# Kernel optimization log

Hardware: AMD Instinct MI355X
Metric: run time of the kernel (lower is better)

Reference implementation:

```python
import jax, jax.numpy as jnp
import numpy as np

B, C, N, K = 2, 128, 8192, 16
DL = 128  # dim_L; Fourier half-dim = 64; mlp hidden = 32


def setup_inputs() -> dict:
    key = jax.random.key(0)
    ks = jax.random.split(key, 16)
    s = 0.05
    return {
        "x": jax.random.normal(ks[0], (B, C, N, 1), jnp.float32),
        "coords": jax.random.normal(ks[1], (B, N, 4), jnp.float32),
        "idx": jax.random.randint(ks[2], (B, N, K), 0, N, jnp.int64),
        "B_gauss": jax.random.normal(ks[3], (4, DL // 2), jnp.float32),
        "W1": jax.random.normal(ks[4], (DL, DL // 4), jnp.float32) * s,
        "b1": jax.random.normal(ks[5], (DL // 4,), jnp.float32) * s,
        "W2": jax.random.normal(ks[6], (DL // 4, C), jnp.float32) * s,
        "b2": jax.random.normal(ks[7], (C,), jnp.float32) * s,
        "Wq": jax.random.normal(ks[8], (C, C), jnp.float32) * s,
        "bq": jax.random.normal(ks[9], (C,), jnp.float32) * s,
        "Wk": jax.random.normal(ks[10], (C, C), jnp.float32) * s,
        "bk": jax.random.normal(ks[11], (C,), jnp.float32) * s,
        "Wv": jax.random.normal(ks[12], (C, C), jnp.float32) * s,
        "bv": jax.random.normal(ks[13], (C,), jnp.float32) * s,
        "Wo": jax.random.normal(ks[14], (C, C), jnp.float32) * s,
        "bo": jax.random.normal(ks[15], (C,), jnp.float32) * s,
    }


def reference(x, coords, idx, B_gauss, W1, b1, W2, b2, Wq, bq, Wk, bk, Wv, bv, Wo, bo):
    xs = x[..., 0]  # [B, C, N]
    # gather neighbor coords/features via KNN idx (vmapped over batch)
    nb_coords = jax.vmap(lambda c, i: c[i])(coords, idx)          # [B, N, K, 4]
    nb_feats = jax.vmap(lambda f, i: f[:, i])(xs, idx)            # [B, C, N, K]
    delta_p = nb_coords - coords[:, :, None, :]                   # [B, N, K, 4]
    # random-Fourier geometric embedding
    proj = jnp.matmul(delta_p, B_gauss)                           # [B, N, K, DL/2]
    two_pi = 2.0 * jnp.pi
    E_freq = jnp.concatenate([jnp.sin(two_pi * proj), jnp.cos(two_pi * proj)], axis=-1)
    h = jax.nn.relu(E_freq @ W1 + b1) @ W2 + b2                   # [B, N, K, C]
    E_geo = jnp.transpose(h, (0, 3, 1, 2))                        # [B, C, N, K]
    # 1x1 conv projections == channel matmuls (PyTorch conv weight acts as out<-in)
    Q = jnp.einsum('oc,bcn->bon', Wq, xs) + bq[None, :, None]     # [B, C, N]
    KV_in = nb_feats + E_geo                                      # [B, C, N, K]
    Kt = jnp.einsum('oc,bcnk->bonk', Wk, KV_in) + bk[None, :, None, None]
    Vt = jnp.einsum('oc,bcnk->bonk', Wv, KV_in) + bv[None, :, None, None]
    # local dot-product attention over K neighbors
    attn = jnp.sum(Q[..., None] * Kt, axis=1, keepdims=True) / jnp.sqrt(jnp.float32(C))
    attn = jax.nn.softmax(attn, axis=-1)                          # [B, 1, N, K]
    out = jnp.sum(attn * Vt, axis=-1, keepdims=True)              # [B, C, N, 1]
    out = jnp.einsum('oc,bcnk->bonk', Wo, out) + bo[None, :, None, None]
    return out
```

## Files before the change

### kernel.cpp

```cpp
#include <hip/hip_runtime.h>


using u16 = unsigned short;
using u32 = unsigned int;
using u64 = unsigned long long;

typedef short bf16x8 __attribute__((ext_vector_type(8)));
typedef float f32x4  __attribute__((ext_vector_type(4)));

__device__ __forceinline__ float bl(u32 u) { return __uint_as_float(u << 16); }
__device__ __forceinline__ float bh(u32 u) { return __uint_as_float(u & 0xffff0000u); }
__device__ __forceinline__ float b2f(u16 u) { return __uint_as_float(((u32)u) << 16); }
__device__ __forceinline__ u16 f2b(float f) {
    u32 u = __float_as_uint(f);
    u32 r = u + 0x7fffu + ((u >> 16) & 1u);
    return (u16)(r >> 16);
}
__device__ __forceinline__ float dot8(uint4 wv, const float* xp) {
    float4 a = *(const float4*)xp;
    float4 b = *(const float4*)(xp + 4);
    return bl(wv.x)*a.x + bh(wv.x)*a.y + bl(wv.y)*a.z + bh(wv.y)*a.w
         + bl(wv.z)*b.x + bh(wv.z)*b.y + bl(wv.w)*b.z + bh(wv.w)*b.w;
}
__device__ __forceinline__ u64 pack4(float a, float b, float c, float d) {
    return (u64)f2b(a) | ((u64)f2b(b) << 16) | ((u64)f2b(c) << 32) | ((u64)f2b(d) << 48);
}
__device__ __forceinline__ int fidxA(int m, int c) {
    return (((m >> 4)*4 + (c >> 5))*64 + ((c >> 3) & 3)*16 + (m & 15))*8 + (c & 7);
}

__global__ void __launch_bounds__(512)
k_pt(const float* __restrict__ x,
     const float* __restrict__ Wq, const float* __restrict__ bq,
     const float* __restrict__ Wk, const float* __restrict__ bk,
     const float* __restrict__ Wv, const float* __restrict__ bv,
     const float* __restrict__ Wo, const float* __restrict__ bo,
     const float* __restrict__ W1, const float* __restrict__ W2,
     u16* __restrict__ Afrag, u16* __restrict__ Wovfrag,
     u16* __restrict__ W1frag, u16* __restrict__ W2frag,
     u16* __restrict__ W2Tfrag,
     float* __restrict__ bA, float* __restrict__ su,
     float* __restrict__ bov, float* __restrict__ d0,
     u16* __restrict__ xT)
{
    const int blk = blockIdx.x, tid = threadIdx.x;

    if (blk >= 130) {
        __shared__ u16 tile[32][33];
        const int blk2 = blk - 130;
        const int b  = blk2 >> 10;
        const int ct = (blk2 >> 8) & 3;
        const int nt = blk2 & 255;
        const int tx = tid & 31, ty = tid >> 5;
        const size_t xb = (size_t)b * 128 * 8192;
        #pragma unroll
        for (int j = 0; j < 2; ++j) {
            int c = ct*32 + ty + j*16;
            tile[ty + j*16][tx] = f2b(x[xb + (size_t)c * 8192 + (size_t)(nt*32 + tx)]);
        }
        __syncthreads();
        #pragma unroll
        for (int j = 0; j < 2; ++j) {
            int n = nt*32 + ty + j*16;
            xT[xb + (size_t)n * 128 + (size_t)(ct*32 + tx)] = tile[tx][ty + j*16];
        }
        return;
    }

    const int i = tid & 127, p = tid >> 7;
    if (blk < 128) {
        __shared__ float sWk[128], sWo[128];
        __shared__ float s_pA[4][128], s_pV[4][128];
        if (tid < 128) sWk[tid] = Wk[tid*128 + blk];
        else if (tid < 256) sWo[tid-128] = Wo[blk*128 + (tid-128)];
        __syncthreads();
        float accA = 0.f, accV = 0.f;
        #pragma unroll 8
        for (int o = p*32; o < p*32 + 32; ++o) {
            accA += sWk[o] * Wq[o*128 + i];
            accV += sWo[o] * Wv[o*128 + i];
        }
        s_pA[p][i] = accA; s_pV[p][i] = accV;
        __syncthreads();
        if (tid < 128) {
            float v = s_pA[0][tid] + s_pA[1][tid] + s_pA[2][tid] + s_pA[3][tid];
            Afrag[fidxA(blk, tid)] = f2b(v);
        } else if (tid < 256) {
            int ii = tid - 128;
            float v = s_pV[0][ii] + s_pV[1][ii] + s_pV[2][ii] + s_pV[3][ii];
            Wovfrag[fidxA(blk, ii)] = f2b(v);
        }
    } else if (blk == 128) {
        __shared__ float s_r[3][4][128];
        float a1 = 0.f, a2 = 0.f, a3 = 0.f;
        #pragma unroll 8
        for (int o = p*32; o < p*32 + 32; ++o) {
            a1 += Wk[o*128 + i] * bq[o];
            a2 += Wq[o*128 + i] * bk[o];
            a3 += Wo[i*128 + o] * bv[o];
        }
        s_r[0][p][i] = a1; s_r[1][p][i] = a2; s_r[2][p][i] = a3;
        __syncthreads();
        if (tid < 128) {
            bA[tid] = s_r[0][0][tid] + s_r[0][1][tid] + s_r[0][2][tid] + s_r[0][3][tid];
        } else if (tid < 256) {
            int ii = tid - 128;
            su[ii] = s_r[1][0][ii] + s_r[1][1][ii] + s_r[1][2][ii] + s_r[1][3][ii];
        } else if (tid < 384) {
            int ii = tid - 256;
            bov[ii] = s_r[2][0][ii] + s_r[2][1][ii] + s_r[2][2][ii] + s_r[2][3][ii] + bo[ii];
        } else if (tid < 448) {
            int l = tid - 384;
            float part = bq[l]*bk[l] + bq[l+64]*bk[l+64];
            part += __shfl_xor(part, 1);
            part += __shfl_xor(part, 2);
            part += __shfl_xor(part, 4);
            part += __shfl_xor(part, 8);
            part += __shfl_xor(part, 16);
            part += __shfl_xor(part, 32);
            if (l == 0) *d0 = part;
        }
    } else {
        for (int e = tid; e < 4096; e += 512) {
            int ii = e & 127, r2 = e >> 7;
            {
                int nt = r2 >> 4, lmm = r2 & 15;
                int ks = ii >> 5, q = (ii >> 3) & 3, j = ii & 7;
                W1frag[((nt*4 + ks)*64 + q*16 + lmm)*8 + j] = f2b(W1[ii*32 + r2]);
            }
            {
                int mt = r2 >> 4, lmm = r2 & 15;
                int ks = ii >> 5, q = (ii >> 3) & 3, j = ii & 7;
                W2frag[((mt*4 + ks)*64 + q*16 + lmm)*8 + j] = f2b(W2[r2*128 + ii]);
            }
            {
                int mt = ii >> 4, lmm = ii & 15;
                int q = r2 >> 3, j = r2 & 7;
                W2Tfrag[(mt*64 + q*16 + lmm)*8 + j] = f2b(W2[r2*128 + ii]);
            }
        }
    }
}

__global__ void __launch_bounds__(256, 4)
k_main(const u16* __restrict__ xT, const float* __restrict__ coords,
       const int* __restrict__ idx, const float* __restrict__ Bg,
       const float* __restrict__ b1g, const float* __restrict__ b2g,
       const u16* __restrict__ Afrag, const u16* __restrict__ Wovfrag,
       const u16* __restrict__ W1frag, const u16* __restrict__ W2frag,
       const u16* __restrict__ W2Tfrag,
       const float* __restrict__ bAg, const float* __restrict__ sug,
       const float* __restrict__ bovg, const float* __restrict__ d0g,
       float* __restrict__ out)
{
    __shared__ __align__(16) u16   sH[128][40];
    __shared__ __align__(16) u16   s_qkb[8][136];
    __shared__ __align__(16) u16   s_gb[8][40];
    __shared__ __align__(16) u16   s_wtb[8][136];
    __shared__ __align__(16) float s_xb[8][132];
    __shared__ __align__(16) float s_del[128][4];
    __shared__ float s_sc[8][17];
    __shared__ float s_attn[8][17];
    __shared__ u16   sHbar[32][12];
    __shared__ float s_e0[8];
    __shared__ __align__(16) float s_b2[128], s_su[128];
    __shared__ float s_bA[128], s_bov[128], s_b1[32];
    __shared__ __align__(16) float sBgT[64][4];
    __shared__ int s_idx[128];

    const int tid = threadIdx.x;
    const int w = tid >> 6, l = tid & 63, lm = l & 15, lq = l >> 4, lmm = lm & 7;
    const int g0 = blockIdx.x * 8;
    const int bsel = g0 >> 13;
    const int n0 = g0 & 8191;
    const size_t bbase = ((size_t)bsel) << 13;
    const float inv_sqrtC = 0.08838834764831845f;

    if (tid < 128) {
        s_bA[tid] = bAg[tid]; s_su[tid] = sug[tid];
        s_bov[tid] = bovg[tid]; s_b2[tid] = b2g[tid];
    } else if (tid < 160) {
        s_b1[tid-128] = b1g[tid-128];
    }
    sBgT[tid >> 2][tid & 3] = Bg[(tid & 3)*64 + (tid >> 2)];
    const float c_d0 = *d0g;

    if (tid < 128) {
        int j = idx[(size_t)g0*16 + tid];
        s_idx[tid] = j;
        float4 cj = *(const float4*)&coords[(size_t)(bbase + j)*4];
        float4 cn = *(const float4*)&coords[(size_t)(g0 + (tid >> 4))*4];
        *(float4*)s_del[tid] = make_float4(cj.x-cn.x, cj.y-cn.y, cj.z-cn.z, cj.w-cn.w);
    }
    f32x4 accq[2] = {{0.f,0.f,0.f,0.f},{0.f,0.f,0.f,0.f}};
    {
        const bf16x8* Af = (const bf16x8*)Afrag;
        bf16x8 bfr[4];
        #pragma unroll
        for (int ks = 0; ks < 4; ++ks)
            bfr[ks] = *(const bf16x8*)&xT[(((size_t)(g0 + lmm)) << 7) + ks*32 + lq*8];
        #pragma unroll
        for (int mi = 0; mi < 2; ++mi) {
            const int ct = w*2 + mi;
            #pragma unroll
            for (int ks = 0; ks < 4; ++ks) {
                bf16x8 a = Af[(ct*4 + ks)*64 + l];
                accq[mi] = __builtin_amdgcn_mfma_f32_16x16x32_bf16(a, bfr[ks], accq[mi], 0, 0, 0);
            }
        }
    }
    __syncthreads();

    if (lm < 8) {
        #pragma unroll
        for (int mi = 0; mi < 2; ++mi) {
            int c0 = (w*2 + mi)*16 + lq*4;
            *(u64*)&s_qkb[lm][c0] = pack4(accq[mi][0] + s_bA[c0],   accq[mi][1] + s_bA[c0+1],
                                          accq[mi][2] + s_bA[c0+2], accq[mi][3] + s_bA[c0+3]);
        }
    }
    __syncthreads();

    {
        const bf16x8* W1f = (const bf16x8*)W1frag;
        bf16x8 w1f[2][4];
        #pragma unroll
        for (int nt = 0; nt < 2; ++nt)
            #pragma unroll
            for (int ks = 0; ks < 4; ++ks) w1f[nt][ks] = W1f[(nt*4 + ks)*64 + l];
        #pragma unroll
        for (int mi = 0; mi < 2; ++mi) {
            const int mt = w*2 + mi;
            float4 d = *(const float4*)s_del[mt*16 + lm];
            bf16x8 ea[4];
            #pragma unroll
            for (int ksp = 0; ksp < 2; ++ksp) {
                #pragma unroll
                for (int jp = 0; jp < 4; ++jp) {
                    int f = ksp*32 + lq*8 + jp*2;
                    float4 ga = *(const float4*)sBgT[f];
                    float4 gb = *(const float4*)sBgT[f+1];
                    float p0 = d.x*ga.x + d.y*ga.y + d.z*ga.z + d.w*ga.w;
                    float p1 = d.x*gb.x + d.y*gb.y + d.z*gb.z + d.w*gb.w;
                    p0 -= floorf(p0); p1 -= floorf(p1);
                    ((u32*)&ea[ksp])[jp]   = (u32)f2b(__builtin_amdgcn_sinf(p0))
                                           | ((u32)f2b(__builtin_amdgcn_sinf(p1)) << 16);
                    ((u32*)&ea[ksp+2])[jp] = (u32)f2b(__builtin_amdgcn_cosf(p0))
                                           | ((u32)f2b(__builtin_amdgcn_cosf(p1)) << 16);
                }
            }
            f32x4 acch[2] = {{0.f,0.f,0.f,0.f},{0.f,0.f,0.f,0.f}};
            #pragma unroll
            for (int ks = 0; ks < 4; ++ks) {
                acch[0] = __builtin_amdgcn_mfma_f32_16x16x32_bf16(ea[ks], w1f[0][ks], acch[0], 0,0,0);
                acch[1] = __builtin_amdgcn_mfma_f32_16x16x32_bf16(ea[ks], w1f[1][ks], acch[1], 0,0,0);
            }
            #pragma unroll
            for (int nt = 0; nt < 2; ++nt) {
                float b1v = s_b1[nt*16 + lm];
                #pragma unroll
                for (int r = 0; r < 4; ++r)
                    sH[mt*16 + lq*4 + r][nt*16 + lm] = f2b(fmaxf(acch[nt][r] + b1v, 0.f));
            }
        }
    }
    if (w < 2) {
        const bf16x8* W2f = (const bf16x8*)W2frag;
        f32x4 accg = {0.f,0.f,0.f,0.f};
        #pragma unroll
        for (int ks = 0; ks < 4; ++ks) {
            bf16x8 a = W2f[(w*4 + ks)*64 + l];
            bf16x8 bv = *(const bf16x8*)&s_qkb[lmm][ks*32 + lq*8];
            accg = __builtin_amdgcn_mfma_f32_16x16x32_bf16(a, bv, accg, 0, 0, 0);
        }
        if (lm < 8) {
            int m0 = w*16 + lq*4;
            *(u64*)&s_gb[lm][m0] = pack4(accg[0], accg[1], accg[2], accg[3]);
        }
    } else {
        int t = tid - 128;
        if (t < 64) {
            int n = t >> 3, sub = t & 7, c0 = sub*16;
            uint4 q0 = *(const uint4*)&s_qkb[n][c0];
            uint4 q1 = *(const uint4*)&s_qkb[n][c0+8];
            uint4 x0 = *(const uint4*)&xT[(((size_t)(g0 + n)) << 7) + c0];
            uint4 x1 = *(const uint4*)&xT[(((size_t)(g0 + n)) << 7) + c0 + 8];
            float part = dot8(q0, &s_b2[c0]) + dot8(q1, &s_b2[c0+8])
                       + dot8(x0, &s_su[c0]) + dot8(x1, &s_su[c0+8]);
            part += __shfl_xor(part, 1);
            part += __shfl_xor(part, 2);
            part += __shfl_xor(part, 4);
            if (sub == 0) s_e0[n] = part + c_d0;
        }
    }
    __syncthreads();

    {
        bf16x8 bq4[5];
        #pragma unroll
        for (int ks = 0; ks < 4; ++ks) bq4[ks] = *(const bf16x8*)&s_qkb[lmm][ks*32 + lq*8];
        bq4[4] = *(const bf16x8*)&s_gb[lmm][lq*8];
        #pragma unroll
        for (int mi = 0; mi < 2; ++mi) {
            const int mt = w*2 + mi;
            const size_t rb = ((size_t)(bbase + s_idx[mt*16 + lm])) << 7;
            f32x4 acc = {0.f,0.f,0.f,0.f};
            #pragma unroll
            for (int ks = 0; ks < 4; ++ks) {
                bf16x8 a = *(const bf16x8*)&xT[rb + ks*32 + lq*8];
                acc = __builtin_amdgcn_mfma_f32_16x16x32_bf16(a, bq4[ks], acc, 0, 0, 0);
            }
            {
                bf16x8 a = *(const bf16x8*)&sH[mt*16 + lm][lq*8];
                acc = __builtin_amdgcn_mfma_f32_16x16x32_bf16(a, bq4[4], acc, 0, 0, 0);
            }
            if (lm == mt) {
                #pragma unroll
                for (int r = 0; r < 4; ++r) s_sc[mt][lq*4 + r] = acc[r];
            }
        }
    }
    __syncthreads();

    if (tid < 128) {
        int n = tid >> 4, k = tid & 15;
        float s = (s_sc[n][k] + s_e0[n]) * inv_sqrtC;
        float mx = s;
        mx = fmaxf(mx, __shfl_xor(mx, 1, 16));
        mx = fmaxf(mx, __shfl_xor(mx, 2, 16));
        mx = fmaxf(mx, __shfl_xor(mx, 4, 16));
        mx = fmaxf(mx, __shfl_xor(mx, 8, 16));
        float ex = __expf(s - mx);
        float sm = ex;
        sm += __shfl_xor(sm, 1, 16);
        sm += __shfl_xor(sm, 2, 16);
        sm += __shfl_xor(sm, 4, 16);
        sm += __shfl_xor(sm, 8, 16);
        s_attn[n][k] = ex / sm;
    }
    __syncthreads();

    {
        int n = tid >> 5, cs = tid & 31, c0 = cs*4;
        float a0[16];
        #pragma unroll
        for (int k = 0; k < 16; ++k) a0[k] = s_attn[n][k];
        float4 facc = *(const float4*)&s_b2[c0];
        #pragma unroll
        for (int k = 0; k < 16; ++k) {
            uint2 v = *(const uint2*)&xT[(((size_t)(bbase + s_idx[n*16 + k])) << 7) + c0];
            facc.x += a0[k]*bl(v.x); facc.y += a0[k]*bh(v.x);
            facc.z += a0[k]*bl(v.y); facc.w += a0[k]*bh(v.y);
        }
        *(float4*)&s_xb[n][c0] = facc;
        int m = cs;
        float hacc = 0.f;
        #pragma unroll
        for (int k = 0; k < 16; ++k) hacc += a0[k] * b2f(sH[n*16 + k][m]);
        sHbar[m][n] = f2b(hacc);
    }
    __syncthreads();

    {
        const bf16x8* W2Tf = (const bf16x8*)W2Tfrag;
        bf16x8 bv;
        #pragma unroll
        for (int j = 0; j < 8; ++j) bv[j] = (short)sHbar[lq*8 + j][lmm];
        #pragma unroll
        for (int mi = 0; mi < 2; ++mi) {
            const int mt = w*2 + mi;
            bf16x8 a = W2Tf[mt*64 + l];
            f32x4 accw = {0.f,0.f,0.f,0.f};
            accw = __builtin_amdgcn_mfma_f32_16x16x32_bf16(a, bv, accw, 0, 0, 0);
            if (lm < 8) {
                int c0 = mt*16 + lq*4;
                float4 xb4 = *(const float4*)&s_xb[lm][c0];
                *(u64*)&s_wtb[lm][c0] = pack4(xb4.x + accw[0], xb4.y + accw[1],
                                              xb4.z + accw[2], xb4.w + accw[3]);
            }
        }
    }
    __syncthreads();

    {
        const bf16x8* Wvf = (const bf16x8*)Wovfrag;
        bf16x8 bv[4];
        #pragma unroll
        for (int ks = 0; ks < 4; ++ks) bv[ks] = *(const bf16x8*)&s_wtb[lmm][ks*32 + lq*8];
        #pragma unroll
        for (int mi = 0; mi < 2; ++mi) {
            const int ct = w*2 + mi;
            f32x4 acco = {0.f,0.f,0.f,0.f};
            #pragma unroll
            for (int ks = 0; ks < 4; ++ks) {
                bf16x8 a = Wvf[(ct*4 + ks)*64 + l];
                acco = __builtin_amdgcn_mfma_f32_16x16x32_bf16(a, bv[ks], acco, 0, 0, 0);
            }
            if (lm < 8) {
                #pragma unroll
                for (int r = 0; r < 4; ++r) {
                    int o = ct*16 + lq*4 + r;
                    out[(((size_t)(bsel*128 + o)) << 13) + n0 + lm] = acco[r] + s_bov[o];
                }
            }
        }
    }
}

extern "C" void kernel_launch(void* const* d_in, const int* in_sizes, int n_in,
                              void* d_out, int out_size, void* d_ws, size_t ws_size,
                              hipStream_t stream)
{
    const float* x      = (const float*)d_in[0];
    const float* coords = (const float*)d_in[1];
    const int*   idx    = (const int*)d_in[2];
    const float* Bg     = (const float*)d_in[3];
    const float* W1     = (const float*)d_in[4];
    const float* b1     = (const float*)d_in[5];
    const float* W2     = (const float*)d_in[6];
    const float* b2     = (const float*)d_in[7];
    const float* Wq     = (const float*)d_in[8];
    const float* bq     = (const float*)d_in[9];
    const float* Wk     = (const float*)d_in[10];
    const float* bk     = (const float*)d_in[11];
    const float* Wv     = (const float*)d_in[12];
    const float* bv     = (const float*)d_in[13];
    const float* Wo     = (const float*)d_in[14];
    const float* bo     = (const float*)d_in[15];
    float* out = (float*)d_out;

    char* ws = (char*)d_ws;
    u16*   Afrag   = (u16*)(ws);
    u16*   Wovfrag = (u16*)(ws + 32768);
    u16*   W1frag  = (u16*)(ws + 65536);
    u16*   W2frag  = (u16*)(ws + 73728);
    u16*   W2Tfrag = (u16*)(ws + 81920);
    float* bA      = (float*)(ws + 90112);
    float* su      = (float*)(ws + 90624);
    float* bov     = (float*)(ws + 91136);
    float* d0      = (float*)(ws + 91648);
    u16*   xT      = (u16*)(ws + 94208);

    k_pt<<<2178, 512, 0, stream>>>(x, Wq, bq, Wk, bk, Wv, bv, Wo, bo, W1, W2,
                                   Afrag, Wovfrag, W1frag, W2frag, W2Tfrag,
                                   bA, su, bov, d0, xT);
    k_main<<<2048, 256, 0, stream>>>(xT, coords, idx, Bg, b1, b2,
                                     Afrag, Wovfrag, W1frag, W2frag, W2Tfrag,
                                     bA, su, bov, d0, out);
}
```

Before: 128.9 us.

## Fold b2 and W2 into precomputed weights, prefetch neighbor rows, fuse softmax

Bias b2 is folded algebraically into the key-side and output constants, and Wo·Wv is premultiplied with W2 into a new fragment matrix. This removes the separate W2^T MFMA stage and one block-wide barrier in the main kernel. Neighbor feature rows are prefetched into registers at kernel start. Softmax is now computed directly from MFMA accumulators with cross-lane shuffles, dropping the score staging buffer and another barrier. Shared-memory bias staging is replaced by direct global reads, blocks interleave the two batches, and the weighted-sum intermediate is stored in bf16, which adds some rounding error.

```diff
diff --git a/kernel.cpp b/kernel.cpp
--- a/kernel.cpp
+++ b/kernel.cpp
@@ -36,11 +36,12 @@
      const float* __restrict__ Wv, const float* __restrict__ bv,
      const float* __restrict__ Wo, const float* __restrict__ bo,
      const float* __restrict__ W1, const float* __restrict__ W2,
+     const float* __restrict__ b2,
      u16* __restrict__ Afrag, u16* __restrict__ Wovfrag,
      u16* __restrict__ W1frag, u16* __restrict__ W2frag,
-     u16* __restrict__ W2Tfrag,
-     float* __restrict__ bA, float* __restrict__ su,
-     float* __restrict__ bov, float* __restrict__ d0,
+     u16* __restrict__ Wovt2frag,
+     float* __restrict__ bA, float* __restrict__ su2,
+     float* __restrict__ bov2, float* __restrict__ d0b,
      u16* __restrict__ xT)
 {
     const int blk = blockIdx.x, tid = threadIdx.x;
@@ -71,6 +72,7 @@
     if (blk < 128) {
         __shared__ float sWk[128], sWo[128];
         __shared__ float s_pA[4][128], s_pV[4][128];
+        __shared__ float s_row[128];
         if (tid < 128) sWk[tid] = Wk[tid*128 + blk];
         else if (tid < 256) sWo[tid-128] = Wo[blk*128 + (tid-128)];
         __syncthreads();
@@ -89,36 +91,51 @@
             int ii = tid - 128;
             float v = s_pV[0][ii] + s_pV[1][ii] + s_pV[2][ii] + s_pV[3][ii];
             Wovfrag[fidxA(blk, ii)] = f2b(v);
+            s_row[ii] = v;
+        }
+        __syncthreads();
+        if (tid < 32) {
+            float wv2 = 0.f;
+            for (int c = 0; c < 128; ++c) wv2 += s_row[c] * W2[tid*128 + c];
+            Wovt2frag[(((blk >> 4)*64) + (tid >> 3)*16 + (blk & 15))*8 + (tid & 7)] = f2b(wv2);
+        } else if (tid == 32) {
+            float rb2 = 0.f, a3 = 0.f;
+            for (int c = 0; c < 128; ++c) rb2 += s_row[c] * b2[c];
+            for (int o = 0; o < 128; ++o) a3 += sWo[o] * bv[o];
+            bov2[blk] = rb2 + a3 + bo[blk];
         }
     } else if (blk == 128) {
-        __shared__ float s_r[3][4][128];
-        float a1 = 0.f, a2 = 0.f, a3 = 0.f;
+        __shared__ float s_t[128];
+        __shared__ float s_p1[4][128], s_p2[4][128];
+        if (tid < 128) {
+            float tt = 0.f;
+            for (int c = 0; c < 128; ++c) tt += Wk[tid*128 + c] * b2[c];
+            s_t[tid] = tt + bk[tid];
+        }
+        __syncthreads();
+        float a1 = 0.f, a2 = 0.f;
         #pragma unroll 8
         for (int o = p*32; o < p*32 + 32; ++o) {
             a1 += Wk[o*128 + i] * bq[o];
-            a2 += Wq[o*128 + i] * bk[o];
-            a3 += Wo[i*128 + o] * bv[o];
-        }
-        s_r[0][p][i] = a1; s_r[1][p][i] = a2; s_r[2][p][i] = a3;
+            a2 += Wq[o*128 + i] * s_t[o];
+        }
+        s_p1[p][i] = a1; s_p2[p][i] = a2;
         __syncthreads();
         if (tid < 128) {
-            bA[tid] = s_r[0][0][tid] + s_r[0][1][tid] + s_r[0][2][tid] + s_r[0][3][tid];
+            bA[tid] = s_p1[0][tid] + s_p1[1][tid] + s_p1[2][tid] + s_p1[3][tid];
         } else if (tid < 256) {
             int ii = tid - 128;
-            su[ii] = s_r[1][0][ii] + s_r[1][1][ii] + s_r[1][2][ii] + s_r[1][3][ii];
-        } else if (tid < 384) {
-            int ii = tid - 256;
-            bov[ii] = s_r[2][0][ii] + s_r[2][1][ii] + s_r[2][2][ii] + s_r[2][3][ii] + bo[ii];
-        } else if (tid < 448) {
-            int l = tid - 384;
-            float part = bq[l]*bk[l] + bq[l+64]*bk[l+64];
+            su2[ii] = s_p2[0][ii] + s_p2[1][ii] + s_p2[2][ii] + s_p2[3][ii];
+        } else if (tid < 320) {
+            int l = tid - 256;
+            float part = bq[l]*s_t[l] + bq[l+64]*s_t[l+64];
             part += __shfl_xor(part, 1);
             part += __shfl_xor(part, 2);
             part += __shfl_xor(part, 4);
             part += __shfl_xor(part, 8);
             part += __shfl_xor(part, 16);
             part += __shfl_xor(part, 32);
-            if (l == 0) *d0 = part;
+            if (l == 0) *d0b = part;
         }
     } else {
         for (int e = tid; e < 4096; e += 512) {
@@ -133,11 +150,6 @@
                 int ks = ii >> 5, q = (ii >> 3) & 3, j = ii & 7;
                 W2frag[((mt*4 + ks)*64 + q*16 + lmm)*8 + j] = f2b(W2[r2*128 + ii]);
             }
-            {
-                int mt = ii >> 4, lmm = ii & 15;
-                int q = r2 >> 3, j = r2 & 7;
-                W2Tfrag[(mt*64 + q*16 + lmm)*8 + j] = f2b(W2[r2*128 + ii]);
-            }
         }
     }
 }
@@ -145,52 +157,57 @@
 __global__ void __launch_bounds__(256, 4)
 k_main(const u16* __restrict__ xT, const float* __restrict__ coords,
        const int* __restrict__ idx, const float* __restrict__ Bg,
-       const float* __restrict__ b1g, const float* __restrict__ b2g,
+       const float* __restrict__ b1g,
        const u16* __restrict__ Afrag, const u16* __restrict__ Wovfrag,
        const u16* __restrict__ W1frag, const u16* __restrict__ W2frag,
-       const u16* __restrict__ W2Tfrag,
-       const float* __restrict__ bAg, const float* __restrict__ sug,
-       const float* __restrict__ bovg, const float* __restrict__ d0g,
+       const u16* __restrict__ Wovt2frag,
+       const float* __restrict__ bAg, const float* __restrict__ su2g,
+       const float* __restrict__ bov2g, const float* __restrict__ d0bg,
        float* __restrict__ out)
 {
     __shared__ __align__(16) u16   sH[128][40];
     __shared__ __align__(16) u16   s_qkb[8][136];
     __shared__ __align__(16) u16   s_gb[8][40];
-    __shared__ __align__(16) u16   s_wtb[8][136];
-    __shared__ __align__(16) float s_xb[8][132];
-    __shared__ __align__(16) float s_del[128][4];
-    __shared__ float s_sc[8][17];
+    __shared__ __align__(16) u16   s_xb[8][136];
+    __shared__ __align__(16) u16   sHbarT[8][40];
     __shared__ float s_attn[8][17];
-    __shared__ u16   sHbar[32][12];
     __shared__ float s_e0[8];
-    __shared__ __align__(16) float s_b2[128], s_su[128];
-    __shared__ float s_bA[128], s_bov[128], s_b1[32];
     __shared__ __align__(16) float sBgT[64][4];
     __shared__ int s_idx[128];
 
     const int tid = threadIdx.x;
     const int w = tid >> 6, l = tid & 63, lm = l & 15, lq = l >> 4, lmm = lm & 7;
-    const int g0 = blockIdx.x * 8;
-    const int bsel = g0 >> 13;
-    const int n0 = g0 & 8191;
+    const int bsel = blockIdx.x & 1;
+    const int n0 = (blockIdx.x >> 1) * 8;
+    const int g0 = (bsel << 13) + n0;
     const size_t bbase = ((size_t)bsel) << 13;
     const float inv_sqrtC = 0.08838834764831845f;
 
-    if (tid < 128) {
-        s_bA[tid] = bAg[tid]; s_su[tid] = sug[tid];
-        s_bov[tid] = bovg[tid]; s_b2[tid] = b2g[tid];
-    } else if (tid < 160) {
-        s_b1[tid-128] = b1g[tid-128];
-    }
     sBgT[tid >> 2][tid & 3] = Bg[(tid & 3)*64 + (tid >> 2)];
-    const float c_d0 = *d0g;
-
-    if (tid < 128) {
-        int j = idx[(size_t)g0*16 + tid];
-        s_idx[tid] = j;
-        float4 cj = *(const float4*)&coords[(size_t)(bbase + j)*4];
-        float4 cn = *(const float4*)&coords[(size_t)(g0 + (tid >> 4))*4];
-        *(float4*)s_del[tid] = make_float4(cj.x-cn.x, cj.y-cn.y, cj.z-cn.z, cj.w-cn.w);
+    const float c_d0b = *d0bg;
+
+    const int r0 = (w*2)*16 + lm, r1 = (w*2 + 1)*16 + lm;
+    const int j0 = idx[(size_t)g0*16 + r0];
+    const int j1 = idx[(size_t)g0*16 + r1];
+    if (lq == 0) { s_idx[r0] = j0; s_idx[r1] = j1; }
+    float4 dA, dB;
+    {
+        float4 cj0 = *(const float4*)&coords[(size_t)(bbase + j0)*4];
+        float4 cn0 = *(const float4*)&coords[(size_t)(g0 + w*2)*4];
+        dA = make_float4(cj0.x-cn0.x, cj0.y-cn0.y, cj0.z-cn0.z, cj0.w-cn0.w);
+        float4 cj1 = *(const float4*)&coords[(size_t)(bbase + j1)*4];
+        float4 cn1 = *(const float4*)&coords[(size_t)(g0 + w*2 + 1)*4];
+        dB = make_float4(cj1.x-cn1.x, cj1.y-cn1.y, cj1.z-cn1.z, cj1.w-cn1.w);
+    }
+    bf16x8 pf[2][4];
+    {
+        const size_t rb0 = ((size_t)(bbase + j0)) << 7;
+        const size_t rb1 = ((size_t)(bbase + j1)) << 7;
+        #pragma unroll
+        for (int ks = 0; ks < 4; ++ks) {
+            pf[0][ks] = *(const bf16x8*)&xT[rb0 + ks*32 + lq*8];
+            pf[1][ks] = *(const bf16x8*)&xT[rb1 + ks*32 + lq*8];
+        }
     }
     f32x4 accq[2] = {{0.f,0.f,0.f,0.f},{0.f,0.f,0.f,0.f}};
     {
@@ -203,20 +220,27 @@
         for (int mi = 0; mi < 2; ++mi) {
             const int ct = w*2 + mi;
             #pragma unroll
-            for (int ks = 0; ks < 4; ++ks) {
-                bf16x8 a = Af[(ct*4 + ks)*64 + l];
-                accq[mi] = __builtin_amdgcn_mfma_f32_16x16x32_bf16(a, bfr[ks], accq[mi], 0, 0, 0);
-            }
-        }
-    }
-    __syncthreads();
-
+            for (int ks = 0; ks < 4; ++ks)
+                accq[mi] = __builtin_amdgcn_mfma_f32_16x16x32_bf16(Af[(ct*4 + ks)*64 + l], bfr[ks], accq[mi], 0, 0, 0);
+        }
+    }
+    if (tid >= 128 && tid < 192) {
+        int t = tid - 128, n = t >> 3, sub = t & 7, c0 = sub*16;
+        uint4 x0 = *(const uint4*)&xT[(((size_t)(g0 + n)) << 7) + c0];
+        uint4 x1 = *(const uint4*)&xT[(((size_t)(g0 + n)) << 7) + c0 + 8];
+        float part = dot8(x0, &su2g[c0]) + dot8(x1, &su2g[c0+8]);
+        part += __shfl_xor(part, 1);
+        part += __shfl_xor(part, 2);
+        part += __shfl_xor(part, 4);
+        if (sub == 0) s_e0[n] = part + c_d0b;
+    }
     if (lm < 8) {
         #pragma unroll
         for (int mi = 0; mi < 2; ++mi) {
             int c0 = (w*2 + mi)*16 + lq*4;
-            *(u64*)&s_qkb[lm][c0] = pack4(accq[mi][0] + s_bA[c0],   accq[mi][1] + s_bA[c0+1],
-                                          accq[mi][2] + s_bA[c0+2], accq[mi][3] + s_bA[c0+3]);
+            float4 bA4 = *(const float4*)&bAg[c0];
+            *(u64*)&s_qkb[lm][c0] = pack4(accq[mi][0] + bA4.x, accq[mi][1] + bA4.y,
+                                          accq[mi][2] + bA4.z, accq[mi][3] + bA4.w);
         }
     }
     __syncthreads();
@@ -228,10 +252,11 @@
         for (int nt = 0; nt < 2; ++nt)
             #pragma unroll
             for (int ks = 0; ks < 4; ++ks) w1f[nt][ks] = W1f[(nt*4 + ks)*64 + l];
+        const float b1a = b1g[lm], b1b = b1g[16 + lm];
         #pragma unroll
         for (int mi = 0; mi < 2; ++mi) {
             const int mt = w*2 + mi;
-            float4 d = *(const float4*)s_del[mt*16 + lm];
+            float4 d = mi ? dB : dA;
             bf16x8 ea[4];
             #pragma unroll
             for (int ksp = 0; ksp < 2; ++ksp) {
@@ -256,11 +281,9 @@
                 acch[1] = __builtin_amdgcn_mfma_f32_16x16x32_bf16(ea[ks], w1f[1][ks], acch[1], 0,0,0);
             }
             #pragma unroll
-            for (int nt = 0; nt < 2; ++nt) {
-                float b1v = s_b1[nt*16 + lm];
-                #pragma unroll
-                for (int r = 0; r < 4; ++r)
-                    sH[mt*16 + lq*4 + r][nt*16 + lm] = f2b(fmaxf(acch[nt][r] + b1v, 0.f));
+            for (int r = 0; r < 4; ++r) {
+                sH[mt*16 + lq*4 + r][lm]      = f2b(fmaxf(acch[0][r] + b1a, 0.f));
+                sH[mt*16 + lq*4 + r][16 + lm] = f2b(fmaxf(acch[1][r] + b1b, 0.f));
             }
         }
     }
@@ -269,29 +292,13 @@
         f32x4 accg = {0.f,0.f,0.f,0.f};
         #pragma unroll
         for (int ks = 0; ks < 4; ++ks) {
-            bf16x8 a = W2f[(w*4 + ks)*64 + l];
             bf16x8 bv = *(const bf16x8*)&s_qkb[lmm][ks*32 + lq*8];
-            accg = __builtin_amdgcn_mfma_f32_16x16x32_bf16(a, bv, accg, 0, 0, 0);
+            accg = __builtin_amdgcn_mfma_f32_16x16x32_bf16(W2f[(w*4 + ks)*64 + l], bv, accg, 0, 0, 0);
         }
         if (lm < 8) {
             int m0 = w*16 + lq*4;
             *(u64*)&s_gb[lm][m0] = pack4(accg[0], accg[1], accg[2], accg[3]);
         }
-    } else {
-        int t = tid - 128;
-        if (t < 64) {
-            int n = t >> 3, sub = t & 7, c0 = sub*16;
-            uint4 q0 = *(const uint4*)&s_qkb[n][c0];
-            uint4 q1 = *(const uint4*)&s_qkb[n][c0+8];
-            uint4 x0 = *(const uint4*)&xT[(((size_t)(g0 + n)) << 7) + c0];
-            uint4 x1 = *(const uint4*)&xT[(((size_t)(g0 + n)) << 7) + c0 + 8];
-            float part = dot8(q0, &s_b2[c0]) + dot8(q1, &s_b2[c0+8])
-                       + dot8(x0, &s_su[c0]) + dot8(x1, &s_su[c0+8]);
-            part += __shfl_xor(part, 1);
-            part += __shfl_xor(part, 2);
-            part += __shfl_xor(part, 4);
-            if (sub == 0) s_e0[n] = part + c_d0;
-        }
     }
     __syncthreads();
 
@@ -303,40 +310,35 @@
         #pragma unroll
         for (int mi = 0; mi < 2; ++mi) {
             const int mt = w*2 + mi;
-            const size_t rb = ((size_t)(bbase + s_idx[mt*16 + lm])) << 7;
             f32x4 acc = {0.f,0.f,0.f,0.f};
             #pragma unroll
-            for (int ks = 0; ks < 4; ++ks) {
-                bf16x8 a = *(const bf16x8*)&xT[rb + ks*32 + lq*8];
-                acc = __builtin_amdgcn_mfma_f32_16x16x32_bf16(a, bq4[ks], acc, 0, 0, 0);
-            }
+            for (int ks = 0; ks < 4; ++ks)
+                acc = __builtin_amdgcn_mfma_f32_16x16x32_bf16(pf[mi][ks], bq4[ks], acc, 0, 0, 0);
             {
                 bf16x8 a = *(const bf16x8*)&sH[mt*16 + lm][lq*8];
                 acc = __builtin_amdgcn_mfma_f32_16x16x32_bf16(a, bq4[4], acc, 0, 0, 0);
             }
+            float e0v = s_e0[mt];
+            float s0 = (acc[0] + e0v) * inv_sqrtC;
+            float s1 = (acc[1] + e0v) * inv_sqrtC;
+            float s2 = (acc[2] + e0v) * inv_sqrtC;
+            float s3 = (acc[3] + e0v) * inv_sqrtC;
+            float mx = fmaxf(fmaxf(s0, s1), fmaxf(s2, s3));
+            mx = fmaxf(mx, __shfl_xor(mx, 16));
+            mx = fmaxf(mx, __shfl_xor(mx, 32));
+            float e0_ = __expf(s0 - mx), e1_ = __expf(s1 - mx);
+            float e2_ = __expf(s2 - mx), e3_ = __expf(s3 - mx);
+            float sm = e0_ + e1_ + e2_ + e3_;
+            sm += __shfl_xor(sm, 16);
+            sm += __shfl_xor(sm, 32);
             if (lm == mt) {
-                #pragma unroll
-                for (int r = 0; r < 4; ++r) s_sc[mt][lq*4 + r] = acc[r];
-            }
-        }
-    }
-    __syncthreads();
-
-    if (tid < 128) {
-        int n = tid >> 4, k = tid & 15;
-        float s = (s_sc[n][k] + s_e0[n]) * inv_sqrtC;
-        float mx = s;
-        mx = fmaxf(mx, __shfl_xor(mx, 1, 16));
-        mx = fmaxf(mx, __shfl_xor(mx, 2, 16));
-        mx = fmaxf(mx, __shfl_xor(mx, 4, 16));
-        mx = fmaxf(mx, __shfl_xor(mx, 8, 16));
-        float ex = __expf(s - mx);
-        float sm = ex;
-        sm += __shfl_xor(sm, 1, 16);
-        sm += __shfl_xor(sm, 2, 16);
-        sm += __shfl_xor(sm, 4, 16);
-        sm += __shfl_xor(sm, 8, 16);
-        s_attn[n][k] = ex / sm;
+                float inv = 1.f / sm;
+                s_attn[mt][lq*4 + 0] = e0_ * inv;
+                s_attn[mt][lq*4 + 1] = e1_ * inv;
+                s_attn[mt][lq*4 + 2] = e2_ * inv;
+                s_attn[mt][lq*4 + 3] = e3_ * inv;
+            }
+        }
     }
     __syncthreads();
 
@@ -345,62 +347,43 @@
         float a0[16];
         #pragma unroll
         for (int k = 0; k < 16; ++k) a0[k] = s_attn[n][k];
-        float4 facc = *(const float4*)&s_b2[c0];
+        float4 facc = make_float4(0.f, 0.f, 0.f, 0.f);
         #pragma unroll
         for (int k = 0; k < 16; ++k) {
             uint2 v = *(const uint2*)&xT[(((size_t)(bbase + s_idx[n*16 + k])) << 7) + c0];
             facc.x += a0[k]*bl(v.x); facc.y += a0[k]*bh(v.x);
             facc.z += a0[k]*bl(v.y); facc.w += a0[k]*bh(v.y);
         }
-        *(float4*)&s_xb[n][c0] = facc;
-        int m = cs;
+        *(u64*)&s_xb[n][c0] = pack4(facc.x, facc.y, facc.z, facc.w);
         float hacc = 0.f;
         #pragma unroll
-        for (int k = 0; k < 16; ++k) hacc += a0[k] * b2f(sH[n*16 + k][m]);
-        sHbar[m][n] = f2b(hacc);
+        for (int k = 0; k < 16; ++k) hacc += a0[k] * b2f(sH[n*16 + k][cs]);
+        sHbarT[n][cs] = f2b(hacc);
     }
     __syncthreads();
 
     {
-        const bf16x8* W2Tf = (const bf16x8*)W2Tfrag;
-        bf16x8 bv;
-        #pragma unroll
-        for (int j = 0; j < 8; ++j) bv[j] = (short)sHbar[lq*8 + j][lmm];
-        #pragma unroll
-        for (int mi = 0; mi < 2; ++mi) {
-            const int mt = w*2 + mi;
-            bf16x8 a = W2Tf[mt*64 + l];
-            f32x4 accw = {0.f,0.f,0.f,0.f};
-            accw = __builtin_amdgcn_mfma_f32_16x16x32_bf16(a, bv, accw, 0, 0, 0);
-            if (lm < 8) {
-                int c0 = mt*16 + lq*4;
-                float4 xb4 = *(const float4*)&s_xb[lm][c0];
-                *(u64*)&s_wtb[lm][c0] = pack4(xb4.x + accw[0], xb4.y + accw[1],
-                                              xb4.z + accw[2], xb4.w + accw[3]);
-            }
-        }
-    }
-    __syncthreads();
-
-    {
-        const bf16x8* Wvf = (const bf16x8*)Wovfrag;
-        bf16x8 bv[4];
-        #pragma unroll
-        for (int ks = 0; ks < 4; ++ks) bv[ks] = *(const bf16x8*)&s_wtb[lmm][ks*32 + lq*8];
+        const bf16x8* Wvf  = (const bf16x8*)Wovfrag;
+        const bf16x8* Wt2f = (const bf16x8*)Wovt2frag;
+        bf16x8 bx[4];
+        #pragma unroll
+        for (int ks = 0; ks < 4; ++ks) bx[ks] = *(const bf16x8*)&s_xb[lmm][ks*32 + lq*8];
+        bf16x8 bh8 = *(const bf16x8*)&sHbarT[lmm][lq*8];
         #pragma unroll
         for (int mi = 0; mi < 2; ++mi) {
             const int ct = w*2 + mi;
             f32x4 acco = {0.f,0.f,0.f,0.f};
             #pragma unroll
-            for (int ks = 0; ks < 4; ++ks) {
-                bf16x8 a = Wvf[(ct*4 + ks)*64 + l];
-                acco = __builtin_amdgcn_mfma_f32_16x16x32_bf16(a, bv[ks], acco, 0, 0, 0);
-            }
+            for (int ks = 0; ks < 4; ++ks)
+                acco = __builtin_amdgcn_mfma_f32_16x16x32_bf16(Wvf[(ct*4 + ks)*64 + l], bx[ks], acco, 0, 0, 0);
+            acco = __builtin_amdgcn_mfma_f32_16x16x32_bf16(Wt2f[ct*64 + l], bh8, acco, 0, 0, 0);
             if (lm < 8) {
+                float4 bo4 = *(const float4*)&bov2g[ct*16 + lq*4];
+                const float* bo4p = &bo4.x;
                 #pragma unroll
                 for (int r = 0; r < 4; ++r) {
                     int o = ct*16 + lq*4 + r;
-                    out[(((size_t)(bsel*128 + o)) << 13) + n0 + lm] = acco[r] + s_bov[o];
+                    out[(((size_t)(bsel*128 + o)) << 13) + n0 + lm] = acco[r] + bo4p[r];
                 }
             }
         }
@@ -430,21 +413,21 @@
     float* out = (float*)d_out;
 
     char* ws = (char*)d_ws;
-    u16*   Afrag   = (u16*)(ws);
-    u16*   Wovfrag = (u16*)(ws + 32768);
-    u16*   W1frag  = (u16*)(ws + 65536);
-    u16*   W2frag  = (u16*)(ws + 73728);
-    u16*   W2Tfrag = (u16*)(ws + 81920);
-    float* bA      = (float*)(ws + 90112);
-    float* su      = (float*)(ws + 90624);
-    float* bov     = (float*)(ws + 91136);
-    float* d0      = (float*)(ws + 91648);
-    u16*   xT      = (u16*)(ws + 94208);
-
-    k_pt<<<2178, 512, 0, stream>>>(x, Wq, bq, Wk, bk, Wv, bv, Wo, bo, W1, W2,
-                                   Afrag, Wovfrag, W1frag, W2frag, W2Tfrag,
-                                   bA, su, bov, d0, xT);
-    k_main<<<2048, 256, 0, stream>>>(xT, coords, idx, Bg, b1, b2,
-                                     Afrag, Wovfrag, W1frag, W2frag, W2Tfrag,
-                                     bA, su, bov, d0, out);
-}
+    u16*   Afrag    = (u16*)(ws);
+    u16*   Wovfrag  = (u16*)(ws + 32768);
+    u16*   W1frag   = (u16*)(ws + 65536);
+    u16*   W2frag   = (u16*)(ws + 73728);
+    u16*   Wovt2frag= (u16*)(ws + 81920);
+    float* bA       = (float*)(ws + 90112);
+    float* su2      = (float*)(ws + 90624);
+    float* bov2     = (float*)(ws + 91136);
+    float* d0b      = (float*)(ws + 91648);
+    u16*   xT       = (u16*)(ws + 94208);
+
+    k_pt<<<2178, 512, 0, stream>>>(x, Wq, bq, Wk, bk, Wv, bv, Wo, bo, W1, W2, b2,
+                                   Afrag, Wovfrag, W1frag, W2frag, Wovt2frag,
+                                   bA, su2, bov2, d0b, xT);
+    k_main<<<2048, 256, 0, stream>>>(xT, coords, idx, Bg, b1,
+                                     Afrag, Wovfrag, W1frag, W2frag, Wovt2frag,
+                                     bA, su2, bov2, d0b, out);
+}
```

New measurement: 159.6 us. 23.8% more time.
